# Performance work log

Measured on AMD Instinct MI355X. Metric: run time of the kernel, lower is better.

Reference implementation:

```python
import jax, jax.numpy as jnp
import numpy as np

N_MESH = 40962
N_GRID = 262144
N_EDGE = 786432
D = 128       # node/edge feature dim
H = 256       # MLP hidden dim
EPS = 1e-5


def _layernorm(x, g, b):
    m = jnp.mean(x, axis=-1, keepdims=True)
    v = jnp.mean(jnp.square(x - m), axis=-1, keepdims=True)
    return (x - m) * jax.lax.rsqrt(v + EPS) * g + b


def _mlp(x, W1, b1, W2, b2, g, beta):
    # Linear -> SiLU -> Linear -> LayerNorm (hidden_layers=1)
    h = jax.nn.silu(x @ W1 + b1)
    return _layernorm(h @ W2 + b2, g, beta)


def setup_inputs() -> dict:
    key = jax.random.key(0)
    ks = jax.random.split(key, 20)
    s = 0.02
    inp = {
        "m2g_efeat": jax.random.normal(ks[0], (N_EDGE, D), jnp.float32),
        "grid_nfeat": jax.random.normal(ks[1], (N_GRID, D), jnp.float32),
        "mesh_nfeat": jax.random.normal(ks[2], (N_MESH, D), jnp.float32),
        "src_idx": jax.random.randint(ks[3], (N_EDGE,), 0, N_MESH, jnp.int32),
        "dst_idx": jax.random.randint(ks[4], (N_EDGE,), 0, N_GRID, jnp.int32),
        # edge MLP: concat(efeat, src, dst) [3D] -> H -> D, LayerNorm
        "eW1": jax.random.normal(ks[5], (3 * D, H), jnp.float32) * s,
        "eb1": jnp.zeros((H,), jnp.float32),
        "eW2": jax.random.normal(ks[6], (H, D), jnp.float32) * s,
        "eb2": jnp.zeros((D,), jnp.float32),
        "eg": jnp.ones((D,), jnp.float32),
        "ebeta": jnp.zeros((D,), jnp.float32),
        # node MLP: concat(agg_efeat, grid_nfeat) [2D] -> H -> D, LayerNorm
        "nW1": jax.random.normal(ks[7], (2 * D, H), jnp.float32) * s,
        "nb1": jnp.zeros((H,), jnp.float32),
        "nW2": jax.random.normal(ks[8], (H, D), jnp.float32) * s,
        "nb2": jnp.zeros((D,), jnp.float32),
        "ng": jnp.ones((D,), jnp.float32),
        "nbeta": jnp.zeros((D,), jnp.float32),
    }
    return inp


def reference(m2g_efeat, grid_nfeat, mesh_nfeat, src_idx, dst_idx,
              eW1, eb1, eW2, eb2, eg, ebeta,
              nW1, nb1, nW2, nb2, ng, nbeta):
    # --- edge MLP (MeshGraphEdgeMLPConcat): gather src/dst, concat, MLP ---
    cat_e = jnp.concatenate(
        [m2g_efeat, mesh_nfeat[src_idx], grid_nfeat[dst_idx]], axis=-1)  # [E, 3D]
    efeat = _mlp(cat_e, eW1, eb1, eW2, eb2, eg, ebeta)                   # [E, D]
    # --- aggregate_and_concat: scatter-sum to dst nodes, concat dst feats ---
    agg = jax.ops.segment_sum(efeat, dst_idx, num_segments=N_GRID)       # [N_grid, D]
    cat_n = jnp.concatenate([agg, grid_nfeat], axis=-1)                  # [N_grid, 2D]
    # --- node MLP + residual ---
    return _mlp(cat_n, nW1, nb1, nW2, nb2, ng, nbeta) + grid_nfeat
```

## Files before the change

kernel.cpp:

```cpp
#include <hip/hip_runtime.h>
#include <hip/hip_bf16.h>

typedef __bf16 bf16_t;
typedef bf16_t bf16x8 __attribute__((ext_vector_type(8)));
typedef float f32x16 __attribute__((ext_vector_type(16)));

#define MFMA32(a, b, c) __builtin_amdgcn_mfma_f32_32x32x16_bf16(a, b, c, 0, 0, 0)

static constexpr int E_EDGE = 786432;
static constexpr int N_GRID = 262144;

static constexpr int E_LDT = 136;
static constexpr int E_ATB = 64 * E_LDT * 2;
static constexpr int E_LDH = 264;
static constexpr int E_LDO = 132;
static constexpr int E_OFF_IDX = 2 * E_ATB;
static constexpr int E_SMEM = E_OFF_IDX + 3 * 256;

static constexpr int LDT = 136;
static constexpr int ATB = 128 * LDT * 2;
static constexpr int LDH = 264;
static constexpr int LDO = 132;
static constexpr int OFF_IDX = 2 * ATB;
static constexpr int SMEM_SZ = OFF_IDX + 3 * 512;

__device__ __forceinline__ void lds_barrier() {
    asm volatile("s_waitcnt lgkmcnt(0)" ::: "memory");
    __builtin_amdgcn_s_barrier();
    __builtin_amdgcn_sched_barrier(0);
}

__device__ __forceinline__ float fast_silu(float x) {
    return x * __builtin_amdgcn_rcpf(1.f + __expf(-x));
}

__global__ void pack_w1(const float* __restrict__ w, bf16_t* __restrict__ out, int tsteps) {
    const int gid = blockIdx.x * 256 + threadIdx.x;
    if (gid >= tsteps * 8 * 8 * 64) return;
    const int lane = gid & 63, grp = gid >> 6;
    const int wave = grp & 7, ks = (grp >> 3) & 7, t = grp >> 6;
    const int n = wave * 32 + (lane & 31);
    const int kb = t * 128 + ks * 16 + (lane >> 5) * 8;
    union { bf16_t h[8]; uint4 u; } pk;
#pragma unroll
    for (int j = 0; j < 8; ++j) pk.h[j] = (bf16_t)w[(size_t)(kb + j) * 256 + n];
    reinterpret_cast<uint4*>(out)[gid] = pk.u;
}

__global__ void pack_w2(const float* __restrict__ w, bf16_t* __restrict__ out) {
    const int gid = blockIdx.x * 256 + threadIdx.x;
    if (gid >= 16 * 4 * 64) return;
    const int lane = gid & 63, grp = gid >> 6;
    const int wn = grp & 3, ks = grp >> 2;
    const int n = wn * 32 + (lane & 31);
    const int kb = ks * 16 + (lane >> 5) * 8;
    union { bf16_t h[8]; uint4 u; } pk;
#pragma unroll
    for (int j = 0; j < 8; ++j) pk.h[j] = (bf16_t)w[(size_t)(kb + j) * 128 + n];
    reinterpret_cast<uint4*>(out)[gid] = pk.u;
}

__global__ void f32_to_bf16_vec(const float* __restrict__ in, bf16_t* __restrict__ out, int n8) {
    int i = blockIdx.x * 256 + threadIdx.x;
    if (i < n8) {
        const float4* p = reinterpret_cast<const float4*>(in + (size_t)i * 8);
        const float4 a = p[0], b = p[1];
        union { bf16_t h[8]; uint4 u; } pk;
        pk.h[0] = (bf16_t)a.x; pk.h[1] = (bf16_t)a.y; pk.h[2] = (bf16_t)a.z; pk.h[3] = (bf16_t)a.w;
        pk.h[4] = (bf16_t)b.x; pk.h[5] = (bf16_t)b.y; pk.h[6] = (bf16_t)b.z; pk.h[7] = (bf16_t)b.w;
        reinterpret_cast<uint4*>(out)[i] = pk.u;
    }
}

__global__ void k_hist(const int* __restrict__ dst, int* __restrict__ deg, int E) {
    int i = blockIdx.x * 256 + threadIdx.x;
    if (i < E) atomicAdd(&deg[dst[i]], 1);
}

__global__ void k_scan1(const int* __restrict__ deg, int* __restrict__ excl,
                        int* __restrict__ bsum) {
    __shared__ int sd[256];
    const int b = blockIdx.x, t = threadIdx.x;
    int4 v = reinterpret_cast<const int4*>(deg)[b * 256 + t];
    const int s0 = v.x, s1 = s0 + v.y, s2 = s1 + v.z, s3 = s2 + v.w;
    sd[t] = s3;
    __syncthreads();
    for (int off = 1; off < 256; off <<= 1) {
        int val = (t >= off) ? sd[t - off] : 0;
        __syncthreads();
        if (t >= off) sd[t] += val;
        __syncthreads();
    }
    const int pre = (t > 0) ? sd[t - 1] : 0;
    int4 o;
    o.x = pre; o.y = pre + s0; o.z = pre + s1; o.w = pre + s2;
    reinterpret_cast<int4*>(excl)[b * 256 + t] = o;
    if (t == 255) bsum[b] = sd[255];
}

__global__ void k_scan2(const int* __restrict__ bsum, int* __restrict__ bofs) {
    __shared__ int sd[256];
    const int t = threadIdx.x;
    sd[t] = bsum[t];
    __syncthreads();
    for (int off = 1; off < 256; off <<= 1) {
        int val = (t >= off) ? sd[t - off] : 0;
        __syncthreads();
        if (t >= off) sd[t] += val;
        __syncthreads();
    }
    bofs[t] = (t > 0) ? sd[t - 1] : 0;
}

__global__ void k_scan3(const int* __restrict__ excl, const int* __restrict__ bofs,
                        int* __restrict__ rowptr, int* __restrict__ cursor, int N, int E) {
    int i = blockIdx.x * 256 + threadIdx.x;
    if (i < N) {
        const int v = excl[i] + bofs[i >> 10];
        rowptr[i] = v;
        cursor[i] = v;
    }
    if (i == 0) rowptr[N] = E;
}

__global__ void k_slot(const int* __restrict__ dst, int* __restrict__ cursor,
                       int* __restrict__ slot, int E) {
    int i = blockIdx.x * 256 + threadIdx.x;
    if (i < E) slot[i] = atomicAdd(&cursor[dst[i]], 1);
}

__global__ __launch_bounds__(512) void k_agg(const bf16_t* __restrict__ efs,
                                             const int* __restrict__ rowptr,
                                             bf16_t* __restrict__ aggb) {
    const int node = blockIdx.x * 32 + (threadIdx.x >> 4);
    const int j = (threadIdx.x & 15) * 8;
    const int beg = rowptr[node], end = rowptr[node + 1];
    float s[8];
#pragma unroll
    for (int i = 0; i < 8; ++i) s[i] = 0.f;
    for (int e = beg; e < end; ++e) {
        bf16x8 v = *reinterpret_cast<const bf16x8*>(efs + (size_t)e * 128 + j);
#pragma unroll
        for (int i = 0; i < 8; ++i) s[i] += (float)v[i];
    }
    union { bf16_t h[8]; uint4 u; } pk;
#pragma unroll
    for (int i = 0; i < 8; ++i) pk.h[i] = (bf16_t)s[i];
    *reinterpret_cast<uint4*>(aggb + (size_t)node * 128 + j) = pk.u;
}

__global__ __launch_bounds__(512, 6) void edge_mlp(
    const float* __restrict__ m2g,
    const bf16_t* __restrict__ gridb, const bf16_t* __restrict__ meshb,
    const int* __restrict__ src_idx, const int* __restrict__ dst_idx,
    const int* __restrict__ slot,
    const bf16_t* __restrict__ W1P,
    const float* __restrict__ b1,
    const bf16_t* __restrict__ W2P,
    const float* __restrict__ b2,
    const float* __restrict__ g, const float* __restrict__ beta,
    bf16_t* __restrict__ efs) {
    __shared__ __align__(16) char smem[E_SMEM];

    const int tid = threadIdx.x;
    const int wave = tid >> 6, lane = tid & 63;
    const int l31 = lane & 31, lk = lane >> 5;
    const int wm = wave >> 2, wn = wave & 3;
    const int r0 = blockIdx.x * 64;
    const int srow = tid >> 3, sc = (tid & 7) * 16;

    int* sidx = (int*)(smem + E_OFF_IDX);
    int* didx = sidx + 64;
    int* slotl = didx + 64;
    if (tid < 64) sidx[tid] = src_idx[r0 + tid];
    else if (tid < 128) didx[tid - 64] = dst_idx[r0 + tid - 64];
    else if (tid < 192) slotl[tid - 128] = slot[r0 + tid - 128];
    lds_barrier();

    bf16_t* buf0 = (bf16_t*)smem;
    bf16_t* buf1 = (bf16_t*)(smem + E_ATB);

    {
        float4 f0[4];
        const float* p0 = m2g + (size_t)(r0 + srow) * 128 + sc;
#pragma unroll
        for (int j = 0; j < 4; ++j) f0[j] = *reinterpret_cast<const float4*>(p0 + j * 4);
        bf16_t* dst = buf0 + srow * E_LDT + sc;
#pragma unroll
        for (int q = 0; q < 2; ++q) {
            union { bf16_t h[8]; uint4 u; } pk;
            const float4 v0 = f0[q * 2], v1 = f0[q * 2 + 1];
            pk.h[0] = (bf16_t)v0.x; pk.h[1] = (bf16_t)v0.y;
            pk.h[2] = (bf16_t)v0.z; pk.h[3] = (bf16_t)v0.w;
            pk.h[4] = (bf16_t)v1.x; pk.h[5] = (bf16_t)v1.y;
            pk.h[6] = (bf16_t)v1.z; pk.h[7] = (bf16_t)v1.w;
            *reinterpret_cast<uint4*>(dst + q * 8) = pk.u;
        }
    }
    uint4 a1[2];
    {
        const bf16_t* p1 = meshb + (size_t)sidx[srow] * 128 + sc;
        a1[0] = *reinterpret_cast<const uint4*>(p1);
        a1[1] = *reinterpret_cast<const uint4*>(p1 + 8);
    }
    lds_barrier();

    f32x16 acc[2] = {};
    auto COMPUTE = [&](const bf16_t* A, int t) {
#pragma unroll
        for (int ks = 0; ks < 8; ++ks) {
            const bf16x8 bw = *reinterpret_cast<const bf16x8*>(
                W1P + ((size_t)((t * 8 + ks) * 8 + wave) * 64 + lane) * 8);
            const int kb = ks * 16 + lk * 8;
            bf16x8 a[2];
#pragma unroll
            for (int mt = 0; mt < 2; ++mt)
                a[mt] = *reinterpret_cast<const bf16x8*>(A + (mt * 32 + l31) * E_LDT + kb);
#pragma unroll
            for (int mt = 0; mt < 2; ++mt)
                acc[mt] = MFMA32(a[mt], bw, acc[mt]);
        }
    };

    uint4 a2[2];
    {
        const bf16_t* p2 = gridb + (size_t)didx[srow] * 128 + sc;
        a2[0] = *reinterpret_cast<const uint4*>(p2);
        a2[1] = *reinterpret_cast<const uint4*>(p2 + 8);
    }
    {
        bf16_t* dst = buf1 + srow * E_LDT + sc;
        *reinterpret_cast<uint4*>(dst) = a1[0];
        *reinterpret_cast<uint4*>(dst + 8) = a1[1];
    }
    COMPUTE(buf0, 0);
    lds_barrier();
    {
        bf16_t* dst = buf0 + srow * E_LDT + sc;
        *reinterpret_cast<uint4*>(dst) = a2[0];
        *reinterpret_cast<uint4*>(dst + 8) = a2[1];
    }
    COMPUTE(buf1, 1);
    lds_barrier();
    COMPUTE(buf0, 2);
    lds_barrier();

    bf16_t* hT = (bf16_t*)smem;
    {
        const int col = wave * 32 + l31;
        const float bb = b1[col];
#pragma unroll
        for (int mt = 0; mt < 2; ++mt)
#pragma unroll
            for (int r = 0; r < 16; ++r) {
                const int row = mt * 32 + (r & 3) + 8 * (r >> 2) + 4 * lk;
                hT[row * E_LDH + col] = (bf16_t)fast_silu(acc[mt][r] + bb);
            }
    }
    lds_barrier();

    f32x16 acc2 = {};
#pragma unroll
    for (int ks = 0; ks < 16; ++ks) {
        const bf16x8 bw = *reinterpret_cast<const bf16x8*>(
            W2P + ((size_t)(ks * 4 + wn) * 64 + lane) * 8);
        const int kb = ks * 16 + lk * 8;
        const bf16x8 a = *reinterpret_cast<const bf16x8*>(hT + (wm * 32 + l31) * E_LDH + kb);
        acc2 = MFMA32(a, bw, acc2);
    }
    lds_barrier();

    float* outl = (float*)smem;
    {
        const int col = wn * 32 + l31;
        const float bb = b2[col];
#pragma unroll
        for (int r = 0; r < 16; ++r) {
            const int row = wm * 32 + (r & 3) + 8 * (r >> 2) + 4 * lk;
            outl[row * E_LDO + col] = acc2[r] + bb;
        }
    }
    lds_barrier();

    {
        const int lrow = tid >> 3, lq = (tid & 7) * 16;
        const float* rpd = outl + lrow * E_LDO + lq;
        float s = 0.f, sq2 = 0.f;
#pragma unroll
        for (int q = 0; q < 4; ++q) {
            const float4 v = *reinterpret_cast<const float4*>(rpd + q * 4);
            s += v.x + v.y + v.z + v.w;
            sq2 += v.x * v.x + v.y * v.y + v.z * v.z + v.w * v.w;
        }
        s += __shfl_xor(s, 1);  sq2 += __shfl_xor(sq2, 1);
        s += __shfl_xor(s, 2);  sq2 += __shfl_xor(sq2, 2);
        s += __shfl_xor(s, 4);  sq2 += __shfl_xor(sq2, 4);
        const float mean = s * (1.f / 128.f);
        const float var = sq2 * (1.f / 128.f) - mean * mean;
        const float rstd = rsqrtf(var + 1e-5f);

        const int sl = slotl[lrow];
        bf16_t* op = efs + (size_t)sl * 128 + lq;
        union { bf16_t h[16]; uint4 u[2]; } pk;
#pragma unroll
        for (int q = 0; q < 4; ++q) {
            const float4 v = *reinterpret_cast<const float4*>(rpd + q * 4);
            const float4 gv = *reinterpret_cast<const float4*>(g + lq + q * 4);
            const float4 bv = *reinterpret_cast<const float4*>(beta + lq + q * 4);
            pk.h[q * 4 + 0] = (bf16_t)((v.x - mean) * rstd * gv.x + bv.x);
            pk.h[q * 4 + 1] = (bf16_t)((v.y - mean) * rstd * gv.y + bv.y);
            pk.h[q * 4 + 2] = (bf16_t)((v.z - mean) * rstd * gv.z + bv.z);
            pk.h[q * 4 + 3] = (bf16_t)((v.w - mean) * rstd * gv.w + bv.w);
        }
        *reinterpret_cast<uint4*>(op) = pk.u[0];
        *reinterpret_cast<uint4*>(op + 8) = pk.u[1];
    }
}

template <bool DENSE>
__global__ __launch_bounds__(512, 4) void node_mlp(
    const bf16_t* __restrict__ aggb,
    const bf16_t* __restrict__ efs,
    const int* __restrict__ rowptr,
    const bf16_t* __restrict__ gridb,
    const float* __restrict__ gridf,
    const bf16_t* __restrict__ W1P,
    const float* __restrict__ b1,
    const bf16_t* __restrict__ W2P,
    const float* __restrict__ b2,
    const float* __restrict__ g, const float* __restrict__ beta,
    float* __restrict__ outp) {
    __shared__ __align__(16) char smem[SMEM_SZ];

    const int tid = threadIdx.x;
    const int wave = tid >> 6, lane = tid & 63;
    const int l31 = lane & 31, lk = lane >> 5;
    const int wm = wave >> 2, wn = wave & 3;
    const int r0 = blockIdx.x * 128;
    const int srow = tid >> 2, sc = (tid & 3) * 32;

    bf16_t* buf0 = (bf16_t*)smem;
    bf16_t* buf1 = (bf16_t*)(smem + ATB);
    int* rp = (int*)(smem + OFF_IDX);

    uint4 a0[4];
    if constexpr (DENSE) {
        const bf16_t* p0 = aggb + (size_t)(r0 + srow) * 128 + sc;
#pragma unroll
        for (int j = 0; j < 4; ++j) a0[j] = *reinterpret_cast<const uint4*>(p0 + j * 8);
    } else {
        if (tid < 129) rp[tid] = rowptr[r0 + tid];
        lds_barrier();
        const int beg = rp[srow], end = rp[srow + 1];
        float s[32];
#pragma unroll
        for (int i = 0; i < 32; ++i) s[i] = 0.f;
        for (int e = beg; e < end; ++e) {
            const bf16_t* p = efs + (size_t)e * 128 + sc;
#pragma unroll
            for (int q = 0; q < 4; ++q) {
                bf16x8 v = *reinterpret_cast<const bf16x8*>(p + q * 8);
#pragma unroll
                for (int i = 0; i < 8; ++i) s[q * 8 + i] += (float)v[i];
            }
        }
#pragma unroll
        for (int q = 0; q < 4; ++q) {
            union { bf16_t h[8]; uint4 u; } pk;
#pragma unroll
            for (int i = 0; i < 8; ++i) pk.h[i] = (bf16_t)s[q * 8 + i];
            a0[q] = pk.u;
        }
    }
    {
        bf16_t* dst = buf0 + srow * LDT + sc;
#pragma unroll
        for (int j = 0; j < 4; ++j) *reinterpret_cast<uint4*>(dst + j * 8) = a0[j];
    }
    uint4 a1[4];
    {
        const bf16_t* p1 = gridb + (size_t)(r0 + srow) * 128 + sc;
#pragma unroll
        for (int j = 0; j < 4; ++j) a1[j] = *reinterpret_cast<const uint4*>(p1 + j * 8);
    }
    lds_barrier();

    f32x16 acc[4] = {};
    auto COMPUTE = [&](const bf16_t* A, int t) {
#pragma unroll
        for (int ks = 0; ks < 8; ++ks) {
            const bf16x8 bw = *reinterpret_cast<const bf16x8*>(
                W1P + ((size_t)((t * 8 + ks) * 8 + wave) * 64 + lane) * 8);
            const int kb = ks * 16 + lk * 8;
            bf16x8 a[4];
#pragma unroll
            for (int mt = 0; mt < 4; ++mt)
                a[mt] = *reinterpret_cast<const bf16x8*>(A + (mt * 32 + l31) * LDT + kb);
#pragma unroll
            for (int mt = 0; mt < 4; ++mt)
                acc[mt] = MFMA32(a[mt], bw, acc[mt]);
        }
    };

    {
        bf16_t* dst = buf1 + srow * LDT + sc;
#pragma unroll
        for (int j = 0; j < 4; ++j) *reinterpret_cast<uint4*>(dst + j * 8) = a1[j];
    }
    COMPUTE(buf0, 0);
    lds_barrier();
    COMPUTE(buf1, 1);
    lds_barrier();

    bf16_t* hT = (bf16_t*)smem;
    {
        const int col = wave * 32 + l31;
        const float bb = b1[col];
#pragma unroll
        for (int mt = 0; mt < 4; ++mt)
#pragma unroll
            for (int r = 0; r < 16; ++r) {
                const int row = mt * 32 + (r & 3) + 8 * (r >> 2) + 4 * lk;
                hT[row * LDH + col] = (bf16_t)fast_silu(acc[mt][r] + bb);
            }
    }
    lds_barrier();

    f32x16 acc2[2] = {};
#pragma unroll
    for (int ks = 0; ks < 16; ++ks) {
        const bf16x8 bw = *reinterpret_cast<const bf16x8*>(
            W2P + ((size_t)(ks * 4 + wn) * 64 + lane) * 8);
        const int kb = ks * 16 + lk * 8;
        bf16x8 a[2];
#pragma unroll
        for (int mt = 0; mt < 2; ++mt)
            a[mt] = *reinterpret_cast<const bf16x8*>(hT + (wm * 64 + mt * 32 + l31) * LDH + kb);
#pragma unroll
        for (int mt = 0; mt < 2; ++mt)
            acc2[mt] = MFMA32(a[mt], bw, acc2[mt]);
    }
    lds_barrier();

    float* outl = (float*)smem;
    {
        const int col = wn * 32 + l31;
        const float bb = b2[col];
#pragma unroll
        for (int mt = 0; mt < 2; ++mt)
#pragma unroll
            for (int r = 0; r < 16; ++r) {
                const int row = wm * 64 + mt * 32 + (r & 3) + 8 * (r >> 2) + 4 * lk;
                outl[row * LDO + col] = acc2[mt][r] + bb;
            }
    }
    lds_barrier();

    {
        const int lrow = tid >> 2, lq = (tid & 3) * 32;
        const float* rpd = outl + lrow * LDO + lq;
        float s = 0.f, sq2 = 0.f;
#pragma unroll
        for (int q = 0; q < 8; ++q) {
            const float4 v = *reinterpret_cast<const float4*>(rpd + q * 4);
            s += v.x + v.y + v.z + v.w;
            sq2 += v.x * v.x + v.y * v.y + v.z * v.z + v.w * v.w;
        }
        s += __shfl_xor(s, 1);  sq2 += __shfl_xor(sq2, 1);
        s += __shfl_xor(s, 2);  sq2 += __shfl_xor(sq2, 2);
        const float mean = s * (1.f / 128.f);
        const float var = sq2 * (1.f / 128.f) - mean * mean;
        const float rstd = rsqrtf(var + 1e-5f);

        const float* grp = gridf + (size_t)(r0 + lrow) * 128 + lq;
        float* op = outp + (size_t)(r0 + lrow) * 128 + lq;
#pragma unroll
        for (int q = 0; q < 8; ++q) {
            const float4 v = *reinterpret_cast<const float4*>(rpd + q * 4);
            const float4 gv = *reinterpret_cast<const float4*>(g + lq + q * 4);
            const float4 bv = *reinterpret_cast<const float4*>(beta + lq + q * 4);
            const float4 rr = *reinterpret_cast<const float4*>(grp + q * 4);
            float4 y;
            y.x = (v.x - mean) * rstd * gv.x + bv.x + rr.x;
            y.y = (v.y - mean) * rstd * gv.y + bv.y + rr.y;
            y.z = (v.z - mean) * rstd * gv.z + bv.z + rr.z;
            y.w = (v.w - mean) * rstd * gv.w + bv.w + rr.w;
            *reinterpret_cast<float4*>(op + q * 4) = y;
        }
    }
}

extern "C" void kernel_launch(void* const* d_in, const int* in_sizes, int n_in,
                              void* d_out, int out_size, void* d_ws, size_t ws_size,
                              hipStream_t stream) {
    const float* m2g = (const float*)d_in[0];
    const float* gridf = (const float*)d_in[1];
    const float* meshf = (const float*)d_in[2];
    const int* src_idx = (const int*)d_in[3];
    const int* dst_idx = (const int*)d_in[4];
    const float* eW1 = (const float*)d_in[5];
    const float* eb1 = (const float*)d_in[6];
    const float* eW2 = (const float*)d_in[7];
    const float* eb2 = (const float*)d_in[8];
    const float* eg = (const float*)d_in[9];
    const float* ebeta = (const float*)d_in[10];
    const float* nW1 = (const float*)d_in[11];
    const float* nb1 = (const float*)d_in[12];
    const float* nW2 = (const float*)d_in[13];
    const float* nb2 = (const float*)d_in[14];
    const float* ng = (const float*)d_in[15];
    const float* nbeta = (const float*)d_in[16];
    float* out = (float*)d_out;

    const size_t mesh_elems = (size_t)in_sizes[2];
    const size_t grid_elems = (size_t)N_GRID * 128;
    const size_t efs_elems = (size_t)E_EDGE * 128;

    char* base = (char*)d_ws;
    size_t off = 0;
    auto alloc = [&](size_t bytes) { size_t o = off; off = (off + bytes + 15) & ~(size_t)15; return o; };

    const size_t o_w1e = alloc(192 * 64 * 8 * 2);
    const size_t o_w2e = alloc(64 * 64 * 8 * 2);
    const size_t o_w1n = alloc(128 * 64 * 8 * 2);
    const size_t o_w2n = alloc(64 * 64 * 8 * 2);
    const size_t o_gridb = alloc(grid_elems * 2);
    const size_t o_meshb = alloc(mesh_elems * 2);
    const size_t o_efs = alloc(efs_elems * 2);
    const size_t o_rowptr = alloc((N_GRID + 1) * 4);
    const size_t o_cursor = alloc((size_t)N_GRID * 4);
    const size_t o_slot = alloc((size_t)E_EDGE * 4);
    const size_t o_deg = alloc((size_t)N_GRID * 4);
    const size_t o_excl = alloc((size_t)N_GRID * 4);
    const size_t o_bsum = alloc(256 * 4);
    const size_t o_bofs = alloc(256 * 4);
    const size_t o_aggb = alloc(grid_elems * 2);
    const size_t need_dense = off;

    bf16_t* W1eP = (bf16_t*)(base + o_w1e);
    bf16_t* W2eP = (bf16_t*)(base + o_w2e);
    bf16_t* W1nP = (bf16_t*)(base + o_w1n);
    bf16_t* W2nP = (bf16_t*)(base + o_w2n);
    bf16_t* gridb = (bf16_t*)(base + o_gridb);
    bf16_t* meshb = (bf16_t*)(base + o_meshb);
    bf16_t* efs = (bf16_t*)(base + o_efs);
    int* rowptr = (int*)(base + o_rowptr);
    int* cursor = (int*)(base + o_cursor);
    int* slot = (int*)(base + o_slot);
    int* deg = (int*)(base + o_deg);
    int* excl = (int*)(base + o_excl);
    int* bsum = (int*)(base + o_bsum);
    int* bofs = (int*)(base + o_bofs);
    bf16_t* aggb = (bf16_t*)(base + o_aggb);

    const bool dense = ws_size >= need_dense;

    pack_w1<<<(192 * 64 + 255) / 256, 256, 0, stream>>>(eW1, W1eP, 3);
    pack_w2<<<(64 * 64 + 255) / 256, 256, 0, stream>>>(eW2, W2eP);
    pack_w1<<<(128 * 64 + 255) / 256, 256, 0, stream>>>(nW1, W1nP, 2);
    pack_w2<<<(64 * 64 + 255) / 256, 256, 0, stream>>>(nW2, W2nP);

    const int g8 = (int)(grid_elems / 8), m8 = (int)(mesh_elems / 8);
    f32_to_bf16_vec<<<(g8 + 255) / 256, 256, 0, stream>>>(gridf, gridb, g8);
    f32_to_bf16_vec<<<(m8 + 255) / 256, 256, 0, stream>>>(meshf, meshb, m8);

    hipMemsetAsync(deg, 0, (size_t)N_GRID * 4, stream);
    k_hist<<<(E_EDGE + 255) / 256, 256, 0, stream>>>(dst_idx, deg, E_EDGE);
    k_scan1<<<256, 256, 0, stream>>>(deg, excl, bsum);
    k_scan2<<<1, 256, 0, stream>>>(bsum, bofs);
    k_scan3<<<(N_GRID + 255) / 256, 256, 0, stream>>>(excl, bofs, rowptr, cursor, N_GRID, E_EDGE);
    k_slot<<<(E_EDGE + 255) / 256, 256, 0, stream>>>(dst_idx, cursor, slot, E_EDGE);

    edge_mlp<<<E_EDGE / 64, 512, 0, stream>>>(
        m2g, gridb, meshb, src_idx, dst_idx, slot,
        W1eP, eb1, W2eP, eb2, eg, ebeta, efs);

    if (dense) {
        k_agg<<<N_GRID / 32, 512, 0, stream>>>(efs, rowptr, aggb);
        node_mlp<true><<<N_GRID / 128, 512, 0, stream>>>(
            aggb, nullptr, nullptr, gridb, gridf,
            W1nP, nb1, W2nP, nb2, ng, nbeta, out);
    } else {
        node_mlp<false><<<N_GRID / 128, 512, 0, stream>>>(
            nullptr, efs, rowptr, gridb, gridf,
            W1nP, nb1, W2nP, nb2, ng, nbeta, out);
    }
}
```

Baseline: 672.1 us.

## Fuse edge aggregation into node MLP and shrink node tile to 64 rows

Drops the separate k_agg kernel and the dense aggb buffer, so node_mlp now always sums each node's CSR-sorted edge features itself. The node tile shrinks from 128 to 64 rows, reusing the edge kernel's LDS layout, so each wave has fewer MFMA tiles and twice as many blocks are launched. Launch bounds rise to 8 blocks per CU for both MLP kernels. This removes a kernel launch and a write/read round trip of the aggregate, but makes the irregular gather part of the GEMM kernel and may add register pressure in edge_mlp under the tighter occupancy bound.

```diff
diff --git a/kernel.cpp b/kernel.cpp
--- a/kernel.cpp
+++ b/kernel.cpp
@@ -16,13 +16,6 @@
 static constexpr int E_LDO = 132;
 static constexpr int E_OFF_IDX = 2 * E_ATB;
 static constexpr int E_SMEM = E_OFF_IDX + 3 * 256;
-
-static constexpr int LDT = 136;
-static constexpr int ATB = 128 * LDT * 2;
-static constexpr int LDH = 264;
-static constexpr int LDO = 132;
-static constexpr int OFF_IDX = 2 * ATB;
-static constexpr int SMEM_SZ = OFF_IDX + 3 * 512;
 
 __device__ __forceinline__ void lds_barrier() {
     asm volatile("s_waitcnt lgkmcnt(0)" ::: "memory");
@@ -129,27 +122,7 @@
     if (i < E) slot[i] = atomicAdd(&cursor[dst[i]], 1);
 }
 
-__global__ __launch_bounds__(512) void k_agg(const bf16_t* __restrict__ efs,
-                                             const int* __restrict__ rowptr,
-                                             bf16_t* __restrict__ aggb) {
-    const int node = blockIdx.x * 32 + (threadIdx.x >> 4);
-    const int j = (threadIdx.x & 15) * 8;
-    const int beg = rowptr[node], end = rowptr[node + 1];
-    float s[8];
-#pragma unroll
-    for (int i = 0; i < 8; ++i) s[i] = 0.f;
-    for (int e = beg; e < end; ++e) {
-        bf16x8 v = *reinterpret_cast<const bf16x8*>(efs + (size_t)e * 128 + j);
-#pragma unroll
-        for (int i = 0; i < 8; ++i) s[i] += (float)v[i];
-    }
-    union { bf16_t h[8]; uint4 u; } pk;
-#pragma unroll
-    for (int i = 0; i < 8; ++i) pk.h[i] = (bf16_t)s[i];
-    *reinterpret_cast<uint4*>(aggb + (size_t)node * 128 + j) = pk.u;
-}
-
-__global__ __launch_bounds__(512, 6) void edge_mlp(
+__global__ __launch_bounds__(512, 8) void edge_mlp(
     const float* __restrict__ m2g,
     const bf16_t* __restrict__ gridb, const bf16_t* __restrict__ meshb,
     const int* __restrict__ src_idx, const int* __restrict__ dst_idx,
@@ -317,9 +290,7 @@
     }
 }
 
-template <bool DENSE>
-__global__ __launch_bounds__(512, 4) void node_mlp(
-    const bf16_t* __restrict__ aggb,
+__global__ __launch_bounds__(512, 8) void node_mlp(
     const bf16_t* __restrict__ efs,
     const int* __restrict__ rowptr,
     const bf16_t* __restrict__ gridb,
@@ -330,82 +301,73 @@
     const float* __restrict__ b2,
     const float* __restrict__ g, const float* __restrict__ beta,
     float* __restrict__ outp) {
-    __shared__ __align__(16) char smem[SMEM_SZ];
+    __shared__ __align__(16) char smem[E_SMEM];
 
     const int tid = threadIdx.x;
     const int wave = tid >> 6, lane = tid & 63;
     const int l31 = lane & 31, lk = lane >> 5;
     const int wm = wave >> 2, wn = wave & 3;
-    const int r0 = blockIdx.x * 128;
-    const int srow = tid >> 2, sc = (tid & 3) * 32;
+    const int r0 = blockIdx.x * 64;
+    const int srow = tid >> 3, sc = (tid & 7) * 16;
 
     bf16_t* buf0 = (bf16_t*)smem;
-    bf16_t* buf1 = (bf16_t*)(smem + ATB);
-    int* rp = (int*)(smem + OFF_IDX);
-
-    uint4 a0[4];
-    if constexpr (DENSE) {
-        const bf16_t* p0 = aggb + (size_t)(r0 + srow) * 128 + sc;
-#pragma unroll
-        for (int j = 0; j < 4; ++j) a0[j] = *reinterpret_cast<const uint4*>(p0 + j * 8);
-    } else {
-        if (tid < 129) rp[tid] = rowptr[r0 + tid];
-        lds_barrier();
+    bf16_t* buf1 = (bf16_t*)(smem + E_ATB);
+    int* rp = (int*)(smem + E_OFF_IDX);
+
+    if (tid < 65) rp[tid] = rowptr[r0 + tid];
+    lds_barrier();
+
+    {
         const int beg = rp[srow], end = rp[srow + 1];
-        float s[32];
-#pragma unroll
-        for (int i = 0; i < 32; ++i) s[i] = 0.f;
+        float s[16];
+#pragma unroll
+        for (int i = 0; i < 16; ++i) s[i] = 0.f;
         for (int e = beg; e < end; ++e) {
             const bf16_t* p = efs + (size_t)e * 128 + sc;
-#pragma unroll
-            for (int q = 0; q < 4; ++q) {
-                bf16x8 v = *reinterpret_cast<const bf16x8*>(p + q * 8);
-#pragma unroll
-                for (int i = 0; i < 8; ++i) s[q * 8 + i] += (float)v[i];
+            bf16x8 v0 = *reinterpret_cast<const bf16x8*>(p);
+            bf16x8 v1 = *reinterpret_cast<const bf16x8*>(p + 8);
+#pragma unroll
+            for (int i = 0; i < 8; ++i) {
+                s[i] += (float)v0[i];
+                s[8 + i] += (float)v1[i];
             }
         }
-#pragma unroll
-        for (int q = 0; q < 4; ++q) {
-            union { bf16_t h[8]; uint4 u; } pk;
-#pragma unroll
-            for (int i = 0; i < 8; ++i) pk.h[i] = (bf16_t)s[q * 8 + i];
-            a0[q] = pk.u;
-        }
-    }
-    {
-        bf16_t* dst = buf0 + srow * LDT + sc;
-#pragma unroll
-        for (int j = 0; j < 4; ++j) *reinterpret_cast<uint4*>(dst + j * 8) = a0[j];
-    }
-    uint4 a1[4];
+        union { bf16_t h[16]; uint4 u[2]; } pk;
+#pragma unroll
+        for (int i = 0; i < 16; ++i) pk.h[i] = (bf16_t)s[i];
+        bf16_t* dst = buf0 + srow * E_LDT + sc;
+        *reinterpret_cast<uint4*>(dst) = pk.u[0];
+        *reinterpret_cast<uint4*>(dst + 8) = pk.u[1];
+    }
+    uint4 a1[2];
     {
         const bf16_t* p1 = gridb + (size_t)(r0 + srow) * 128 + sc;
-#pragma unroll
-        for (int j = 0; j < 4; ++j) a1[j] = *reinterpret_cast<const uint4*>(p1 + j * 8);
-    }
-    lds_barrier();
-
-    f32x16 acc[4] = {};
+        a1[0] = *reinterpret_cast<const uint4*>(p1);
+        a1[1] = *reinterpret_cast<const uint4*>(p1 + 8);
+    }
+    lds_barrier();
+
+    f32x16 acc[2] = {};
     auto COMPUTE = [&](const bf16_t* A, int t) {
 #pragma unroll
         for (int ks = 0; ks < 8; ++ks) {
             const bf16x8 bw = *reinterpret_cast<const bf16x8*>(
                 W1P + ((size_t)((t * 8 + ks) * 8 + wave) * 64 + lane) * 8);
             const int kb = ks * 16 + lk * 8;
-            bf16x8 a[4];
-#pragma unroll
-            for (int mt = 0; mt < 4; ++mt)
-                a[mt] = *reinterpret_cast<const bf16x8*>(A + (mt * 32 + l31) * LDT + kb);
-#pragma unroll
-            for (int mt = 0; mt < 4; ++mt)
+            bf16x8 a[2];
+#pragma unroll
+            for (int mt = 0; mt < 2; ++mt)
+                a[mt] = *reinterpret_cast<const bf16x8*>(A + (mt * 32 + l31) * E_LDT + kb);
+#pragma unroll
+            for (int mt = 0; mt < 2; ++mt)
                 acc[mt] = MFMA32(a[mt], bw, acc[mt]);
         }
     };
 
     {
-        bf16_t* dst = buf1 + srow * LDT + sc;
-#pragma unroll
-        for (int j = 0; j < 4; ++j) *reinterpret_cast<uint4*>(dst + j * 8) = a1[j];
+        bf16_t* dst = buf1 + srow * E_LDT + sc;
+        *reinterpret_cast<uint4*>(dst) = a1[0];
+        *reinterpret_cast<uint4*>(dst + 8) = a1[1];
     }
     COMPUTE(buf0, 0);
     lds_barrier();
@@ -417,28 +379,23 @@
         const int col = wave * 32 + l31;
         const float bb = b1[col];
 #pragma unroll
-        for (int mt = 0; mt < 4; ++mt)
+        for (int mt = 0; mt < 2; ++mt)
 #pragma unroll
             for (int r = 0; r < 16; ++r) {
                 const int row = mt * 32 + (r & 3) + 8 * (r >> 2) + 4 * lk;
-                hT[row * LDH + col] = (bf16_t)fast_silu(acc[mt][r] + bb);
+                hT[row * E_LDH + col] = (bf16_t)fast_silu(acc[mt][r] + bb);
             }
     }
     lds_barrier();
 
-    f32x16 acc2[2] = {};
+    f32x16 acc2 = {};
 #pragma unroll
     for (int ks = 0; ks < 16; ++ks) {
         const bf16x8 bw = *reinterpret_cast<const bf16x8*>(
             W2P + ((size_t)(ks * 4 + wn) * 64 + lane) * 8);
         const int kb = ks * 16 + lk * 8;
-        bf16x8 a[2];
-#pragma unroll
-        for (int mt = 0; mt < 2; ++mt)
-            a[mt] = *reinterpret_cast<const bf16x8*>(hT + (wm * 64 + mt * 32 + l31) * LDH + kb);
-#pragma unroll
-        for (int mt = 0; mt < 2; ++mt)
-            acc2[mt] = MFMA32(a[mt], bw, acc2[mt]);
+        const bf16x8 a = *reinterpret_cast<const bf16x8*>(hT + (wm * 32 + l31) * E_LDH + kb);
+        acc2 = MFMA32(a, bw, acc2);
     }
     lds_barrier();
 
@@ -447,27 +404,26 @@
         const int col = wn * 32 + l31;
         const float bb = b2[col];
 #pragma unroll
-        for (int mt = 0; mt < 2; ++mt)
-#pragma unroll
-            for (int r = 0; r < 16; ++r) {
-                const int row = wm * 64 + mt * 32 + (r & 3) + 8 * (r >> 2) + 4 * lk;
-                outl[row * LDO + col] = acc2[mt][r] + bb;
-            }
-    }
-    lds_barrier();
-
-    {
-        const int lrow = tid >> 2, lq = (tid & 3) * 32;
-        const float* rpd = outl + lrow * LDO + lq;
+        for (int r = 0; r < 16; ++r) {
+            const int row = wm * 32 + (r & 3) + 8 * (r >> 2) + 4 * lk;
+            outl[row * E_LDO + col] = acc2[r] + bb;
+        }
+    }
+    lds_barrier();
+
+    {
+        const int lrow = tid >> 3, lq = (tid & 7) * 16;
+        const float* rpd = outl + lrow * E_LDO + lq;
         float s = 0.f, sq2 = 0.f;
 #pragma unroll
-        for (int q = 0; q < 8; ++q) {
+        for (int q = 0; q < 4; ++q) {
             const float4 v = *reinterpret_cast<const float4*>(rpd + q * 4);
             s += v.x + v.y + v.z + v.w;
             sq2 += v.x * v.x + v.y * v.y + v.z * v.z + v.w * v.w;
         }
         s += __shfl_xor(s, 1);  sq2 += __shfl_xor(sq2, 1);
         s += __shfl_xor(s, 2);  sq2 += __shfl_xor(sq2, 2);
+        s += __shfl_xor(s, 4);  sq2 += __shfl_xor(sq2, 4);
         const float mean = s * (1.f / 128.f);
         const float var = sq2 * (1.f / 128.f) - mean * mean;
         const float rstd = rsqrtf(var + 1e-5f);
@@ -475,7 +431,7 @@
         const float* grp = gridf + (size_t)(r0 + lrow) * 128 + lq;
         float* op = outp + (size_t)(r0 + lrow) * 128 + lq;
 #pragma unroll
-        for (int q = 0; q < 8; ++q) {
+        for (int q = 0; q < 4; ++q) {
             const float4 v = *reinterpret_cast<const float4*>(rpd + q * 4);
             const float4 gv = *reinterpret_cast<const float4*>(g + lq + q * 4);
             const float4 bv = *reinterpret_cast<const float4*>(beta + lq + q * 4);
@@ -534,8 +490,6 @@
     const size_t o_excl = alloc((size_t)N_GRID * 4);
     const size_t o_bsum = alloc(256 * 4);
     const size_t o_bofs = alloc(256 * 4);
-    const size_t o_aggb = alloc(grid_elems * 2);
-    const size_t need_dense = off;
 
     bf16_t* W1eP = (bf16_t*)(base + o_w1e);
     bf16_t* W2eP = (bf16_t*)(base + o_w2e);
@@ -551,9 +505,6 @@
     int* excl = (int*)(base + o_excl);
     int* bsum = (int*)(base + o_bsum);
     int* bofs = (int*)(base + o_bofs);
-    bf16_t* aggb = (bf16_t*)(base + o_aggb);
-
-    const bool dense = ws_size >= need_dense;
 
     pack_w1<<<(192 * 64 + 255) / 256, 256, 0, stream>>>(eW1, W1eP, 3);
     pack_w2<<<(64 * 64 + 255) / 256, 256, 0, stream>>>(eW2, W2eP);
@@ -575,14 +526,7 @@
         m2g, gridb, meshb, src_idx, dst_idx, slot,
         W1eP, eb1, W2eP, eb2, eg, ebeta, efs);
 
-    if (dense) {
-        k_agg<<<N_GRID / 32, 512, 0, stream>>>(efs, rowptr, aggb);
-        node_mlp<true><<<N_GRID / 128, 512, 0, stream>>>(
-            aggb, nullptr, nullptr, gridb, gridf,
-            W1nP, nb1, W2nP, nb2, ng, nbeta, out);
-    } else {
-        node_mlp<false><<<N_GRID / 128, 512, 0, stream>>>(
-            nullptr, efs, rowptr, gridb, gridf,
-            W1nP, nb1, W2nP, nb2, ng, nbeta, out);
-    }
-}
+    node_mlp<<<N_GRID / 64, 512, 0, stream>>>(
+        efs, rowptr, gridb, gridf,
+        W1nP, nb1, W2nP, nb2, ng, nbeta, out);
+}
```

After: 616.6 us. -8.3%, faster.
